# Performance work log

Measured on AMD Instinct MI355X. Metric: run time of the kernel, lower is better.

Reference implementation:

```python
import jax, jax.numpy as jnp
import numpy as np

QN = 5.0  # params['mich']['Q_n']
# lb/ub for ['R_1','1/R_1C_1','OCV - U','-M_H','K_H','x','y'] (mich)
LB = jnp.array([0.0, 0.0, 0.05, 0.0, 0.0, 0.04236, 0.023], dtype=jnp.float32)
UB = jnp.array([0.04, 1e-06, 0.8, 0.0, 0.0, 0.84, 0.84804], dtype=jnp.float32)


def ocv_curve_mich(ocv_params):
    x = ocv_params[..., 0:1]
    y = ocv_params[..., 1:2]
    Up = (4.4167 - 1.6518 * y + 1.6225 * y**2 - 2.0843 * y**3 + 3.5146 * y**4
          - 2.2166 * y**5 - 4 * jnp.exp(109.451 * y - 100.006))
    Un = (0.063 + 0.8 * jnp.exp(-75 * (x + 0.001))
          - 0.012 * jnp.tanh((x - 0.127) / 0.016)
          - 0.0118 * jnp.tanh((x - 0.155) / 0.016)
          - 0.0035 * jnp.tanh((x - 0.22) / 0.02)
          - 0.0095 * jnp.tanh((x - 0.19) / 0.013)
          - 0.0145 * jnp.tanh((x - 0.49) / 0.02)
          - 0.08 * jnp.tanh((x - 1.03) / 0.055))
    return Up - Un


def setup_inputs() -> dict:
    key = jax.random.key(0)
    kX, kSC, k1, k2, k3, k4 = jax.random.split(key, 6)
    B, T = 512, 8192
    X = jax.random.normal(kX, (B, T, 3), dtype=jnp.float32)
    SC = jax.random.normal(kSC, (B, 2), dtype=jnp.float32)
    W1 = jax.random.normal(k1, (3, 6), dtype=jnp.float32) * 0.5
    b1 = jax.random.normal(k2, (6,), dtype=jnp.float32) * 0.1
    W2 = jax.random.normal(k3, (6, 7), dtype=jnp.float32) * 0.5
    b2 = jax.random.normal(k4, (7,), dtype=jnp.float32) * 0.1
    return {"X": X, "SC": SC, "W1": W1, "b1": b1, "W2": W2, "b2": b2}


def reference(X, SC, W1, b1, W2, b2):
    t = X[..., 0:1]      # [B,T,1]
    I = X[..., 1:2]      # [B,T,1]
    Temp = X[..., 2:3]   # [B,T,1]
    Q = SC[..., 0:1]     # [B,1]
    R0 = SC[..., 1:2]    # [B,1]

    # Coulomb-counting SOC (trapezoidal), cumulative over time
    dSOC = (I[:, 1:, :] + I[:, :-1, :]) * (t[:, 1:, :] - t[:, :-1, :]) / (2.0 * 3600.0 * QN)
    SOC = jnp.cumsum(jnp.concatenate([jnp.zeros_like(I[:, :1, :]), dSOC], axis=1), axis=1)
    SOC = SOC + Q[:, None, :] / QN  # [B,T,1]

    Tmean = jnp.nanmean(Temp, axis=1, keepdims=True)  # [B,1,1]
    x = jnp.concatenate([SOC,
                         jnp.broadcast_to(R0[:, None, :], SOC.shape),
                         jnp.broadcast_to(Tmean, SOC.shape)], axis=-1)  # [B,T,3]

    h = jax.nn.softplus(x @ W1 + b1)
    p = h @ W2 + b2
    theta = LB + (UB - LB) * jax.nn.sigmoid(0.01 * p)  # [B,T,7]

    R1 = theta[..., 0:1]
    R1C1r = theta[..., 1:2]
    OCV_U = theta[..., 2:3]
    mMH = theta[..., 3:4]
    KH = theta[..., 4:5]
    OCV = ocv_curve_mich(theta[..., 5:])  # [B,T,1]

    # Faithful quirk of source: odeint's t_mask selects channel 0 of
    # X_ode = [I, R_1, 1/R_1C_1, -M_H, K_H], so dt_i = I_{i+1} - I_i.
    dt = I[:, 1:, 0] - I[:, :-1, 0]  # [B, T-1]

    UH0 = jnp.zeros_like(Q)                         # [B,1]
    U10 = -OCV_U[:, 0, :] - UH0 - I[:, 0, :] * R0   # [B,1]
    y0 = jnp.concatenate([UH0, U10], axis=-1)       # [B,2]

    def step(y, inp):
        dti, Ii, R1i, Ci, Mi, Ki = inp
        UH = y[:, 0:1]
        U1 = y[:, 1:2]
        dUH = -Ki * Ii * (-Mi - UH)
        dU1 = Ci * (R1i * Ii - U1)
        ynew = y + dti[:, None] * jnp.concatenate([dUH, dU1], axis=-1)
        return ynew, ynew

    # Euler integration uses params at step i (not i+1): slice [:, :-1, :]
    xs = (dt.T,
          I[:, :-1, :].transpose(1, 0, 2),
          R1[:, :-1, :].transpose(1, 0, 2),
          R1C1r[:, :-1, :].transpose(1, 0, 2),
          mMH[:, :-1, :].transpose(1, 0, 2),
          KH[:, :-1, :].transpose(1, 0, 2))
    _, ys = jax.lax.scan(step, y0, xs)              # ys: [T-1,B,2]
    voltages = jnp.concatenate([y0[None], ys], axis=0).transpose(1, 0, 2)  # [B,T,2]

    UH = voltages[..., 0:1]
    U1 = voltages[..., 1:2]
    pred_U = OCV + UH + U1 + I * R0[:, None, :]     # [B,T,1]
    return pred_U
```

## Files before the change

kernel.cpp:

```cpp
#include <hip/hip_runtime.h>
#include <math.h>


#define TT    8192
#define BLK   1024
#define NW    16
#define EPT   8
#define NNODE 128

__device__ __forceinline__ float frcp(float x) { return __builtin_amdgcn_rcpf(x); }
__device__ __forceinline__ float fsig(float x) { return frcp(1.0f + __expf(-x)); }
__device__ __forceinline__ float ftanh_x(float x) {
    return 1.0f - 2.0f * frcp(__expf(2.0f * x) + 1.0f);
}
__device__ __forceinline__ float fsoftplus_x(float z) {
    return fmaxf(z, 0.0f) + __logf(1.0f + __expf(-fabsf(z)));
}

__device__ __forceinline__ void eval_chain(float soc,
    const float* __restrict__ w1, const float* __restrict__ pre1,
    const float* __restrict__ w2, const float* __restrict__ bb2,
    float& OCV, float& R1, float& C, float& OCVU)
{
    float h[6];
    #pragma unroll
    for (int i = 0; i < 6; ++i)
        h[i] = fsoftplus_x(fmaf(soc, w1[i], pre1[i]));
    float p0 = bb2[0], p1 = bb2[1], p2 = bb2[2], p5 = bb2[5], p6 = bb2[6];
    #pragma unroll
    for (int i = 0; i < 6; ++i) {
        p0 = fmaf(h[i], w2[7*i + 0], p0);
        p1 = fmaf(h[i], w2[7*i + 1], p1);
        p2 = fmaf(h[i], w2[7*i + 2], p2);
        p5 = fmaf(h[i], w2[7*i + 5], p5);
        p6 = fmaf(h[i], w2[7*i + 6], p6);
    }
    R1   = 0.04f * fsig(0.01f * p0);
    C    = 1e-6f * fsig(0.01f * p1);
    OCVU = fmaf(0.75f,    fsig(0.01f * p2), 0.05f);
    float ox = fmaf(0.79764f, fsig(0.01f * p5), 0.04236f);
    float oy = fmaf(0.82504f, fsig(0.01f * p6), 0.023f);
    float up = fmaf(oy, fmaf(oy, fmaf(oy, fmaf(oy, fmaf(oy, -2.2166f, 3.5146f),
                    -2.0843f), 1.6225f), -1.6518f), 4.4167f);
    up -= 4.0f * __expf(fmaf(109.451f, oy, -100.006f));
    float un = 0.063f + 0.8f * __expf(-75.0f * (ox + 0.001f));
    un = fmaf(-0.012f,  ftanh_x((ox - 0.127f) * 62.5f),        un);
    un = fmaf(-0.0118f, ftanh_x((ox - 0.155f) * 62.5f),        un);
    un = fmaf(-0.0035f, ftanh_x((ox - 0.22f)  * 50.0f),        un);
    un = fmaf(-0.0095f, ftanh_x((ox - 0.19f)  * 76.9230769f),  un);
    un = fmaf(-0.0145f, ftanh_x((ox - 0.49f)  * 50.0f),        un);
    un = fmaf(-0.08f,   ftanh_x((ox - 1.03f)  * 18.1818182f),  un);
    OCV = up - un;
}

__global__ void __launch_bounds__(BLK, 4)
voltnet_kernel(const float* __restrict__ X, const float* __restrict__ SC,
               const float* __restrict__ W1, const float* __restrict__ b1,
               const float* __restrict__ W2, const float* __restrict__ b2,
               float* __restrict__ out)
{
    __shared__ float  tw[NW], dw[NW], mnw[NW], mxw[NW], sA[NW], sB[NW];
    __shared__ float4 nodes[NNODE];
    __shared__ float  bcU10;

    const int b    = blockIdx.x;
    const int tid  = threadIdx.x;
    const int lane = tid & 63;
    const int wv   = tid >> 6;
    const int s    = tid * EPT;

    const float* __restrict__ Xrow = X + (size_t)b * TT * 3;
    const float Q  = SC[2 * b + 0];
    const float R0 = SC[2 * b + 1];

    float w1[18], bb1[6], w2[42], bb2[7];
    #pragma unroll
    for (int i = 0; i < 18; ++i) w1[i] = W1[i];
    #pragma unroll
    for (int i = 0; i < 6;  ++i) bb1[i] = b1[i];
    #pragma unroll
    for (int i = 0; i < 42; ++i) w2[i] = W2[i];
    #pragma unroll
    for (int i = 0; i < 7;  ++i) bb2[i] = b2[i];

    float Ireg[EPT], lp[EPT];
    float tsum = 0.0f, run = 0.0f;
    float mnl = 1e30f, mxl = -1e30f;
    float tprev = 0.0f, iprev = 0.0f;
    if (tid > 0) { tprev = Xrow[3 * s - 3]; iprev = Xrow[3 * s - 2]; }
    const float inext_last = (tid < BLK - 1) ? Xrow[3 * (s + EPT) + 1] : 0.0f;

    const float4* __restrict__ Xv = (const float4*)(Xrow + 3 * s);
    #pragma unroll
    for (int c = 0; c < 2; ++c) {
        float4 q0 = Xv[3 * c + 0], q1 = Xv[3 * c + 1], q2 = Xv[3 * c + 2];
        float f[12] = { q0.x, q0.y, q0.z, q0.w, q1.x, q1.y,
                        q1.z, q1.w, q2.x, q2.y, q2.z, q2.w };
        #pragma unroll
        for (int u = 0; u < 4; ++u) {
            int e = 4 * c + u;
            float tt = f[3 * u + 0];
            float ii = f[3 * u + 1];
            float ds = (ii + iprev) * (tt - tprev) * (1.0f / 36000.0f);
            if (e == 0 && tid == 0) ds = 0.0f;
            run += ds;
            lp[e]   = run;
            Ireg[e] = ii;
            mnl = fminf(mnl, run);
            mxl = fmaxf(mxl, run);
            tsum += f[3 * u + 2];
            tprev = tt; iprev = ii;
        }
    }

    float ts = tsum;
    #pragma unroll
    for (int d = 32; d > 0; d >>= 1) ts += __shfl_down(ts, d, 64);
    float inc = run;
    #pragma unroll
    for (int d = 1; d < 64; d <<= 1) {
        float v = __shfl_up(inc, d, 64);
        if (lane >= d) inc += v;
    }
    if (lane == 0)  tw[wv] = ts;
    if (lane == 63) dw[wv] = inc;
    __syncthreads();

    float Tsum = 0.0f;
    #pragma unroll
    for (int w = 0; w < NW; ++w) Tsum += tw[w];
    const float Tmean = Tsum * (1.0f / (float)TT);
    float woff = 0.0f;
    for (int w = 0; w < wv; ++w) woff += dw[w];
    const float soc_base = fmaf(Q, 0.2f, woff + (inc - run));

    float mn_t = soc_base + mnl, mx_t = soc_base + mxl;
    #pragma unroll
    for (int d = 32; d > 0; d >>= 1) {
        mn_t = fminf(mn_t, __shfl_down(mn_t, d, 64));
        mx_t = fmaxf(mx_t, __shfl_down(mx_t, d, 64));
    }
    if (lane == 0) { mnw[wv] = mn_t; mxw[wv] = mx_t; }
    __syncthreads();
    float lo = 1e30f, hi = -1e30f;
    #pragma unroll
    for (int w = 0; w < NW; ++w) { lo = fminf(lo, mnw[w]); hi = fmaxf(hi, mxw[w]); }
    {
        float pad = fmaf(hi - lo, 1.0f / 256.0f, 1e-7f);
        lo -= pad; hi += pad;
    }
    const float hstep = (hi - lo) * (1.0f / (float)(NNODE - 1));
    const float invh  = (float)(NNODE - 1) * frcp(hi - lo);

    float pre1[6];
    #pragma unroll
    for (int o = 0; o < 6; ++o)
        pre1[o] = fmaf(R0, w1[6 + o], fmaf(Tmean, w1[12 + o], bb1[o]));

    if (tid < NNODE) {
        float OCV, R1v, Cv, OCVU;
        eval_chain(fmaf((float)tid, hstep, lo), w1, pre1, w2, bb2, OCV, R1v, Cv, OCVU);
        nodes[tid] = make_float4(OCV, R1v, Cv, 0.0f);
    }
    if (tid == 0) {
        float OCV, R1v, Cv, OCVU;
        eval_chain(soc_base, w1, pre1, w2, bb2, OCV, R1v, Cv, OCVU);
        bcU10 = -OCVU - Ireg[0] * R0;
    }
    __syncthreads();

    float Ap = 1.0f, Bp = 0.0f;
    #pragma unroll
    for (int e = 0; e < EPT; ++e) {
        float soc = soc_base + lp[e];
        float u   = (soc - lo) * invh;
        int   k   = (int)u;
        k = (k < 0) ? 0 : ((k > NNODE - 2) ? NNODE - 2 : k);
        float fr  = u - (float)k;
        float4 n0 = nodes[k];
        float4 n1 = nodes[k + 1];
        float OCV = fmaf(fr, n1.x - n0.x, n0.x);
        float R1v = fmaf(fr, n1.y - n0.y, n0.y);
        float Cv  = fmaf(fr, n1.z - n0.z, n0.z);

        float ii  = Ireg[e];
        float inx = (e == EPT - 1) ? inext_last : Ireg[e + 1];

        lp[e]   = fmaf(ii, R0, OCV) + Bp;
        Ireg[e] = Ap;

        float g  = (inx - ii) * Cv;
        float aj = 1.0f - g;
        float bj = g * R1v * ii;
        if (e == EPT - 1) {
            bool last = (tid == BLK - 1);
            aj = last ? 1.0f : aj;
            bj = last ? 0.0f : bj;
        }
        Bp = fmaf(aj, Bp, bj);
        Ap = aj * Ap;
    }

    float A = Ap, B = Bp;
    #pragma unroll
    for (int d = 1; d < 64; d <<= 1) {
        float Au = __shfl_up(A, d, 64);
        float Bu = __shfl_up(B, d, 64);
        if (lane >= d) { B = fmaf(A, Bu, B); A = A * Au; }
    }
    float Aex = __shfl_up(A, 1, 64);
    float Bex = __shfl_up(B, 1, 64);
    if (lane == 0) { Aex = 1.0f; Bex = 0.0f; }
    if (lane == 63) { sA[wv] = A; sB[wv] = B; }
    __syncthreads();
    float Ao = 1.0f, Bo = 0.0f;
    for (int w = 0; w < wv; ++w) {
        Bo = fmaf(sA[w], Bo, sB[w]);
        Ao = sA[w] * Ao;
    }
    const float U1s = fmaf(Aex * Ao, bcU10, fmaf(Aex, Bo, Bex));

    float4* __restrict__ Ov = (float4*)(out + (size_t)b * TT + s);
    #pragma unroll
    for (int c = 0; c < 2; ++c) {
        float4 o;
        o.x = fmaf(Ireg[4 * c + 0], U1s, lp[4 * c + 0]);
        o.y = fmaf(Ireg[4 * c + 1], U1s, lp[4 * c + 1]);
        o.z = fmaf(Ireg[4 * c + 2], U1s, lp[4 * c + 2]);
        o.w = fmaf(Ireg[4 * c + 3], U1s, lp[4 * c + 3]);
        Ov[c] = o;
    }
}

extern "C" void kernel_launch(void* const* d_in, const int* in_sizes, int n_in,
                              void* d_out, int out_size, void* d_ws, size_t ws_size,
                              hipStream_t stream)
{
    const float* X  = (const float*)d_in[0];
    const float* SC = (const float*)d_in[1];
    const float* W1 = (const float*)d_in[2];
    const float* b1 = (const float*)d_in[3];
    const float* W2 = (const float*)d_in[4];
    const float* b2 = (const float*)d_in[5];
    float* outp = (float*)d_out;
    const int B = in_sizes[1] / 2;
    hipLaunchKernelGGL(voltnet_kernel, dim3(B), dim3(BLK), 0, stream,
                       X, SC, W1, b1, W2, b2, outp);
}
```

Before: 107.9 us.

## Stage row through padded LDS with strided coalesced loads and stores

Halves the block to 512 threads with 16 elements each. Time and current are now loaded with thread-strided coalesced scalar reads into bank-padded shared arrays, replacing the per-thread contiguous float4 loads. The scan phases run on LDS data, and the output is written back in coalesced strided order with nontemporal stores. This adds LDS traffic and extra barriers and uses about 64KB of shared memory per block, which limits blocks per CU, in exchange for better global access patterns.

Measured after the change: 104.2 us. 3.4% less time.

```diff
diff --git a/kernel.cpp b/kernel.cpp
--- a/kernel.cpp
+++ b/kernel.cpp
@@ -3,10 +3,11 @@
 
 
 #define TT    8192
-#define BLK   1024
-#define NW    16
-#define EPT   8
+#define BLK   512
+#define NW    8
+#define EPT   16
 #define NNODE 128
+#define PADJ(j) ((j) + ((j) >> 5))
 
 __device__ __forceinline__ float frcp(float x) { return __builtin_amdgcn_rcpf(x); }
 __device__ __forceinline__ float fsig(float x) { return frcp(1.0f + __expf(-x)); }
@@ -59,8 +60,11 @@
                const float* __restrict__ W2, const float* __restrict__ b2,
                float* __restrict__ out)
 {
+    __shared__ float  ldsT[PADJ(TT - 1) + 2];
+    __shared__ float  ldsI[PADJ(TT - 1) + 2];
     __shared__ float  tw[NW], dw[NW], mnw[NW], mxw[NW], sA[NW], sB[NW];
     __shared__ float4 nodes[NNODE];
+    __shared__ float  U1arr[BLK];
     __shared__ float  bcU10;
 
     const int b    = blockIdx.x;
@@ -83,56 +87,63 @@
     #pragma unroll
     for (int i = 0; i < 7;  ++i) bb2[i] = b2[i];
 
-    float Ireg[EPT], lp[EPT];
-    float tsum = 0.0f, run = 0.0f;
+    float tsum = 0.0f;
+    #pragma unroll 4
+    for (int it = 0; it < EPT; ++it) {
+        int j = tid + it * BLK;
+        float tt = Xrow[3 * j + 0];
+        float ii = Xrow[3 * j + 1];
+        float tp = Xrow[3 * j + 2];
+        ldsT[PADJ(j)] = tt;
+        ldsI[PADJ(j)] = ii;
+        tsum += tp;
+    }
+    #pragma unroll
+    for (int d = 32; d > 0; d >>= 1) tsum += __shfl_down(tsum, d, 64);
+    if (lane == 0) tw[wv] = tsum;
+    __syncthreads();
+
+    float Tsum = 0.0f;
+    #pragma unroll
+    for (int w = 0; w < NW; ++w) Tsum += tw[w];
+    const float Tmean = Tsum * (1.0f / (float)TT);
+
+    float pre1[6];
+    #pragma unroll
+    for (int o = 0; o < 6; ++o)
+        pre1[o] = fmaf(R0, w1[6 + o], fmaf(Tmean, w1[12 + o], bb1[o]));
+
+    float tprev = 0.0f, iprev = 0.0f;
+    if (tid > 0) { tprev = ldsT[PADJ(s - 1)]; iprev = ldsI[PADJ(s - 1)]; }
+    const float inext_last = (tid < BLK - 1) ? ldsI[PADJ(s + EPT)] : 0.0f;
+    __syncthreads();
+
+    float lp = 0.0f;
     float mnl = 1e30f, mxl = -1e30f;
-    float tprev = 0.0f, iprev = 0.0f;
-    if (tid > 0) { tprev = Xrow[3 * s - 3]; iprev = Xrow[3 * s - 2]; }
-    const float inext_last = (tid < BLK - 1) ? Xrow[3 * (s + EPT) + 1] : 0.0f;
-
-    const float4* __restrict__ Xv = (const float4*)(Xrow + 3 * s);
-    #pragma unroll
-    for (int c = 0; c < 2; ++c) {
-        float4 q0 = Xv[3 * c + 0], q1 = Xv[3 * c + 1], q2 = Xv[3 * c + 2];
-        float f[12] = { q0.x, q0.y, q0.z, q0.w, q1.x, q1.y,
-                        q1.z, q1.w, q2.x, q2.y, q2.z, q2.w };
-        #pragma unroll
-        for (int u = 0; u < 4; ++u) {
-            int e = 4 * c + u;
-            float tt = f[3 * u + 0];
-            float ii = f[3 * u + 1];
-            float ds = (ii + iprev) * (tt - tprev) * (1.0f / 36000.0f);
-            if (e == 0 && tid == 0) ds = 0.0f;
-            run += ds;
-            lp[e]   = run;
-            Ireg[e] = ii;
-            mnl = fminf(mnl, run);
-            mxl = fmaxf(mxl, run);
-            tsum += f[3 * u + 2];
-            tprev = tt; iprev = ii;
-        }
-    }
-
-    float ts = tsum;
-    #pragma unroll
-    for (int d = 32; d > 0; d >>= 1) ts += __shfl_down(ts, d, 64);
-    float inc = run;
+    #pragma unroll 4
+    for (int e = 0; e < EPT; ++e) {
+        int j = s + e;
+        float tt = ldsT[PADJ(j)];
+        float ii = ldsI[PADJ(j)];
+        float ds = (ii + iprev) * (tt - tprev) * (1.0f / 36000.0f);
+        if (j == 0) ds = 0.0f;
+        lp += ds;
+        ldsT[PADJ(j)] = lp;
+        mnl = fminf(mnl, lp);
+        mxl = fmaxf(mxl, lp);
+        tprev = tt; iprev = ii;
+    }
+    float inc = lp;
     #pragma unroll
     for (int d = 1; d < 64; d <<= 1) {
         float v = __shfl_up(inc, d, 64);
         if (lane >= d) inc += v;
     }
-    if (lane == 0)  tw[wv] = ts;
     if (lane == 63) dw[wv] = inc;
     __syncthreads();
-
-    float Tsum = 0.0f;
-    #pragma unroll
-    for (int w = 0; w < NW; ++w) Tsum += tw[w];
-    const float Tmean = Tsum * (1.0f / (float)TT);
     float woff = 0.0f;
     for (int w = 0; w < wv; ++w) woff += dw[w];
-    const float soc_base = fmaf(Q, 0.2f, woff + (inc - run));
+    const float soc_base = fmaf(Q, 0.2f, woff + (inc - lp));
 
     float mn_t = soc_base + mnl, mx_t = soc_base + mxl;
     #pragma unroll
@@ -152,11 +163,6 @@
     const float hstep = (hi - lo) * (1.0f / (float)(NNODE - 1));
     const float invh  = (float)(NNODE - 1) * frcp(hi - lo);
 
-    float pre1[6];
-    #pragma unroll
-    for (int o = 0; o < 6; ++o)
-        pre1[o] = fmaf(R0, w1[6 + o], fmaf(Tmean, w1[12 + o], bb1[o]));
-
     if (tid < NNODE) {
         float OCV, R1v, Cv, OCVU;
         eval_chain(fmaf((float)tid, hstep, lo), w1, pre1, w2, bb2, OCV, R1v, Cv, OCVU);
@@ -165,38 +171,35 @@
     if (tid == 0) {
         float OCV, R1v, Cv, OCVU;
         eval_chain(soc_base, w1, pre1, w2, bb2, OCV, R1v, Cv, OCVU);
-        bcU10 = -OCVU - Ireg[0] * R0;
+        bcU10 = -OCVU - ldsI[PADJ(0)] * R0;
     }
     __syncthreads();
 
     float Ap = 1.0f, Bp = 0.0f;
-    #pragma unroll
+    #pragma unroll 4
     for (int e = 0; e < EPT; ++e) {
-        float soc = soc_base + lp[e];
-        float u   = (soc - lo) * invh;
-        int   k   = (int)u;
+        int j = s + e;
+        float soc = soc_base + ldsT[PADJ(j)];
+        float ii  = ldsI[PADJ(j)];
+        float inx = (e == EPT - 1) ? inext_last : ldsI[PADJ(j + 1)];
+
+        float u  = (soc - lo) * invh;
+        int   k  = (int)u;
         k = (k < 0) ? 0 : ((k > NNODE - 2) ? NNODE - 2 : k);
-        float fr  = u - (float)k;
+        float fr = u - (float)k;
         float4 n0 = nodes[k];
         float4 n1 = nodes[k + 1];
         float OCV = fmaf(fr, n1.x - n0.x, n0.x);
         float R1v = fmaf(fr, n1.y - n0.y, n0.y);
         float Cv  = fmaf(fr, n1.z - n0.z, n0.z);
 
-        float ii  = Ireg[e];
-        float inx = (e == EPT - 1) ? inext_last : Ireg[e + 1];
-
-        lp[e]   = fmaf(ii, R0, OCV) + Bp;
-        Ireg[e] = Ap;
+        ldsT[PADJ(j)] = fmaf(ii, R0, OCV) + Bp;
+        ldsI[PADJ(j)] = Ap;
 
         float g  = (inx - ii) * Cv;
         float aj = 1.0f - g;
         float bj = g * R1v * ii;
-        if (e == EPT - 1) {
-            bool last = (tid == BLK - 1);
-            aj = last ? 1.0f : aj;
-            bj = last ? 0.0f : bj;
-        }
+        if (j == TT - 1) { aj = 1.0f; bj = 0.0f; }
         Bp = fmaf(aj, Bp, bj);
         Ap = aj * Ap;
     }
@@ -219,16 +222,15 @@
         Ao = sA[w] * Ao;
     }
     const float U1s = fmaf(Aex * Ao, bcU10, fmaf(Aex, Bo, Bex));
-
-    float4* __restrict__ Ov = (float4*)(out + (size_t)b * TT + s);
-    #pragma unroll
-    for (int c = 0; c < 2; ++c) {
-        float4 o;
-        o.x = fmaf(Ireg[4 * c + 0], U1s, lp[4 * c + 0]);
-        o.y = fmaf(Ireg[4 * c + 1], U1s, lp[4 * c + 1]);
-        o.z = fmaf(Ireg[4 * c + 2], U1s, lp[4 * c + 2]);
-        o.w = fmaf(Ireg[4 * c + 3], U1s, lp[4 * c + 3]);
-        Ov[c] = o;
+    U1arr[tid] = U1s;
+    __syncthreads();
+
+    float* __restrict__ orow = out + (size_t)b * TT;
+    #pragma unroll 4
+    for (int it = 0; it < EPT; ++it) {
+        int j = tid + it * BLK;
+        float v = fmaf(ldsI[PADJ(j)], U1arr[j >> 4], ldsT[PADJ(j)]);
+        __builtin_nontemporal_store(v, &orow[j]);
     }
 }
 
```
